# Kernel tuning notes

Hardware: AMD Instinct MI355X
Metric: run time of the kernel (lower is better)

The kernel has to match this reference:

```python
import jax, jax.numpy as jnp
import numpy as np

TAU = 0.2  # args.gumble_tau


def _segment_softmax(vals, seg, num_seg):
    # torch.sparse.softmax(dim=1): softmax over the nonzero entries of each row
    m = jax.ops.segment_max(vals, seg, num_segments=num_seg)
    e = jnp.exp(vals - m[seg])
    s = jax.ops.segment_sum(e, seg, num_segments=num_seg)
    return e / s[seg]


def _masked_attention(q_embed, k_embed, Wq, bq, Wk, bk, rows, cols, noise, num_rows):
    # Q = self.Q(q_embed); K = self.K(k_embed)
    Q = q_embed @ Wq + bq            # [Nq, H]
    K = k_embed @ Wk + bk            # [Nk, H]
    # sparse_dense_mul(adj, Q @ K.T) -> only gather edge entries (same math)
    w = jnp.sum(Q[rows] * K[cols], axis=-1)   # [E]
    g = jnp.log(-jnp.log(noise))              # gumble_G = log(-log(rand))
    z = (w - g) / TAU
    return _segment_softmax(z, rows, num_rows)


def setup_inputs() -> dict:
    key = jax.random.key(0)
    ks = jax.random.split(key, 10)
    U, I, D, H, E = 50000, 25000, 256, 128, 1600000
    inp = {
        "user_embed": jax.random.normal(ks[0], (U, D), jnp.float32),
        "item_embed": jax.random.normal(ks[1], (I, D), jnp.float32),
        "Wq": jax.random.normal(ks[2], (D, H), jnp.float32) * 0.05,
        "bq": jax.random.normal(ks[3], (H,), jnp.float32) * 0.05,
        "Wk": jax.random.normal(ks[4], (D, H), jnp.float32) * 0.05,
        "bk": jax.random.normal(ks[5], (H,), jnp.float32) * 0.05,
        "ui_rows": jax.random.randint(ks[6], (E,), 0, U, jnp.int32),
        "ui_cols": jax.random.randint(ks[7], (E,), 0, I, jnp.int32),
        "noise_ui": jax.random.uniform(ks[8], (E,), jnp.float32, 1e-6, 1.0),
        "noise_iu": jax.random.uniform(ks[9], (E,), jnp.float32, 1e-6, 1.0),
    }
    return inp


def reference(user_embed, item_embed, Wq, bq, Wk, bk, ui_rows, ui_cols, noise_ui, noise_iu):
    U = user_embed.shape[0]
    I = item_embed.shape[0]
    # M_ui: rows = users, softmax over items per user
    vals_ui = _masked_attention(user_embed, item_embed, Wq, bq, Wk, bk,
                                ui_rows, ui_cols, noise_ui, U)
    # M_iu: transposed adjacency, rows = items, same Q/K layers
    vals_iu = _masked_attention(item_embed, user_embed, Wq, bq, Wk, bk,
                                ui_cols, ui_rows, noise_iu, I)
    # mask values = cat([M_ui.values(), M_iu.values()])
    return jnp.concatenate([vals_ui, vals_iu])
```

## Files before the change

### kernel.cpp

```cpp
#include <hip/hip_runtime.h>
#include <hip/hip_fp16.h>
#include <math.h>

#define TAU_INV 5.0f
#define LOG2E   1.4426950408889634f

typedef _Float16 half2v __attribute__((ext_vector_type(2)));

__device__ __forceinline__ float fast_exp2(float x) { return __builtin_amdgcn_exp2f(x); }
__device__ __forceinline__ float fast_log2(float x) { return __builtin_amdgcn_logf(x); }

__global__ void init_sumd(double* __restrict__ seg_sumd, int n) {
    int i = blockIdx.x * blockDim.x + threadIdx.x;
    if (i < n) seg_sumd[i] = 0.0;
}

__device__ __forceinline__ double exp_double(float z) {
    float y = z * LOG2E;
    float n = rintf(y);
    float r = y - n;
    float f = fast_exp2(r);
    long long e = (long long)n + 1023;
    if (e < 1)    e = 1;
    if (e > 2046) e = 2046;
    double scale = __longlong_as_double(e << 52);
    return (double)f * scale;
}

__device__ __forceinline__ float log2_of_double(double v) {
    unsigned long long b = __double_as_longlong(v);
    int ex = (int)((b >> 52) & 0x7FFULL) - 1023;
    double m = __longlong_as_double((b & 0xFFFFFFFFFFFFFULL) | 0x3FF0000000000000ULL);
    return (float)ex + fast_log2((float)m);
}

__global__ __launch_bounds__(256) void gemm_qk_merged(
    const float* __restrict__ Xu, const float* __restrict__ Xi,
    const float* __restrict__ Wq, const float* __restrict__ bq,
    const float* __restrict__ Wk, const float* __restrict__ bk,
    __half* __restrict__ QK,
    int U, int I, int D)
{
    __shared__ float As_t[16][68];
    __shared__ float Bs_q[16][132];
    __shared__ float Bs_k[16][132];

    const int tid  = threadIdx.x;
    const int row0 = blockIdx.x * 64;
    const int tr   = tid >> 5;
    const int tc   = tid & 31;

    float4 accq[8], acck[8];
#pragma unroll
    for (int i = 0; i < 8; ++i) {
        accq[i] = make_float4(0.f, 0.f, 0.f, 0.f);
        acck[i] = make_float4(0.f, 0.f, 0.f, 0.f);
    }

    const int ar  = tid >> 2;
    const int akq = (tid & 3) * 4;

    for (int k0 = 0; k0 < D; k0 += 16) {
        {
            int gr = row0 + ar;
            float4 v = make_float4(0.f, 0.f, 0.f, 0.f);
            if (gr < U)            v = *(const float4*)&Xu[(size_t)gr * D + k0 + akq];
            else if (gr - U < I)   v = *(const float4*)&Xi[(size_t)(gr - U) * D + k0 + akq];
            As_t[akq + 0][ar] = v.x;
            As_t[akq + 1][ar] = v.y;
            As_t[akq + 2][ar] = v.z;
            As_t[akq + 3][ar] = v.w;
        }
#pragma unroll
        for (int t = 0; t < 2; ++t) {
            int idx = tid + t * 256;
            int r  = idx >> 5;
            int c4 = (idx & 31) * 4;
            float4 vq = *(const float4*)&Wq[(size_t)(k0 + r) * 128 + c4];
            float4 vk = *(const float4*)&Wk[(size_t)(k0 + r) * 128 + c4];
            *(float4*)&Bs_q[r][c4] = vq;
            *(float4*)&Bs_k[r][c4] = vk;
        }
        __syncthreads();

#pragma unroll
        for (int kk = 0; kk < 16; ++kk) {
            float4 a0  = *(const float4*)&As_t[kk][tr * 8];
            float4 a1  = *(const float4*)&As_t[kk][tr * 8 + 4];
            float4 bqv = *(const float4*)&Bs_q[kk][tc * 4];
            float4 bkv = *(const float4*)&Bs_k[kk][tc * 4];
            float a[8] = {a0.x, a0.y, a0.z, a0.w, a1.x, a1.y, a1.z, a1.w};
#pragma unroll
            for (int i = 0; i < 8; ++i) {
                accq[i].x += a[i] * bqv.x;
                accq[i].y += a[i] * bqv.y;
                accq[i].z += a[i] * bqv.z;
                accq[i].w += a[i] * bqv.w;
                acck[i].x += a[i] * bkv.x;
                acck[i].y += a[i] * bkv.y;
                acck[i].z += a[i] * bkv.z;
                acck[i].w += a[i] * bkv.w;
            }
        }
        __syncthreads();
    }

    const float4 bbq = *(const float4*)&bq[tc * 4];
    const float4 bbk = *(const float4*)&bk[tc * 4];
    const int NT = U + I;
#pragma unroll
    for (int i = 0; i < 8; ++i) {
        int gr = row0 + tr * 8 + i;
        if (gr < NT) {
            __half2 q01 = __floats2half2_rn(accq[i].x + bbq.x, accq[i].y + bbq.y);
            __half2 q23 = __floats2half2_rn(accq[i].z + bbq.z, accq[i].w + bbq.w);
            __half2 k01 = __floats2half2_rn(acck[i].x + bbk.x, acck[i].y + bbk.y);
            __half2 k23 = __floats2half2_rn(acck[i].z + bbk.z, acck[i].w + bbk.w);
            uint2 pq, pk;
            pq.x = *(const unsigned int*)&q01;
            pq.y = *(const unsigned int*)&q23;
            pk.x = *(const unsigned int*)&k01;
            pk.y = *(const unsigned int*)&k23;
            *(uint2*)&QK[(size_t)gr * 256 + tc * 4]       = pq;
            *(uint2*)&QK[(size_t)gr * 256 + 128 + tc * 4] = pk;
        }
    }
}

__global__ __launch_bounds__(256) void edge_w_both(
    const __half* __restrict__ QK,
    const int* __restrict__ rows, const int* __restrict__ cols,
    const float* __restrict__ noise_ui, const float* __restrict__ noise_iu,
    float* __restrict__ out, double* __restrict__ seg_sumd, int U, int E)
{
    const int gtid = blockIdx.x * 256 + threadIdx.x;
    const int eid  = gtid >> 3;
    if (eid >= E) return;
    const int hl = threadIdx.x & 7;

    const int r = __builtin_nontemporal_load(&rows[eid]);
    const int c = __builtin_nontemporal_load(&cols[eid]);
    const __half* urow = QK + (size_t)r * 256;
    const __half* irow = QK + (size_t)(U + c) * 256;

    const uint4 qu0 = *(const uint4*)(urow + hl * 16);
    const uint4 qu1 = *(const uint4*)(urow + hl * 16 + 8);
    const uint4 ku0 = *(const uint4*)(urow + 128 + hl * 16);
    const uint4 ku1 = *(const uint4*)(urow + 128 + hl * 16 + 8);
    const uint4 qi0 = *(const uint4*)(irow + hl * 16);
    const uint4 qi1 = *(const uint4*)(irow + hl * 16 + 8);
    const uint4 ki0 = *(const uint4*)(irow + 128 + hl * 16);
    const uint4 ki1 = *(const uint4*)(irow + 128 + hl * 16 + 8);

    float d0 = 0.0f, d1 = 0.0f;
    {
        const half2v* a0 = (const half2v*)&qu0;
        const half2v* b0 = (const half2v*)&ki0;
        const half2v* a1 = (const half2v*)&qi0;
        const half2v* b1 = (const half2v*)&ku0;
#pragma unroll
        for (int t = 0; t < 4; ++t) {
            d0 = __builtin_amdgcn_fdot2(a0[t], b0[t], d0, false);
            d1 = __builtin_amdgcn_fdot2(a1[t], b1[t], d1, false);
        }
        const half2v* a0b = (const half2v*)&qu1;
        const half2v* b0b = (const half2v*)&ki1;
        const half2v* a1b = (const half2v*)&qi1;
        const half2v* b1b = (const half2v*)&ku1;
#pragma unroll
        for (int t = 0; t < 4; ++t) {
            d0 = __builtin_amdgcn_fdot2(a0b[t], b0b[t], d0, false);
            d1 = __builtin_amdgcn_fdot2(a1b[t], b1b[t], d1, false);
        }
    }
    d0 += __shfl_xor(d0, 4);  d1 += __shfl_xor(d1, 4);
    d0 += __shfl_xor(d0, 2);  d1 += __shfl_xor(d1, 2);
    d0 += __shfl_xor(d0, 1);  d1 += __shfl_xor(d1, 1);

    if (hl < 2) {
        const int g  = hl;
        const float d  = g ? d1 : d0;
        const float nz = g ? __builtin_nontemporal_load(&noise_iu[eid])
                           : __builtin_nontemporal_load(&noise_ui[eid]);
        const float zz = (d - __logf(-__logf(nz))) * TAU_INV;
        const int s  = g ? (U + c) : r;
        __builtin_nontemporal_store(zz, &out[(size_t)g * E + eid]);
        atomicAdd(&seg_sumd[s], exp_double(zz));
    }
}

__global__ void edge_norm2v(float* __restrict__ z,
                            const int* __restrict__ rows, const int* __restrict__ cols,
                            const double* __restrict__ seg_sumd, int U, int E)
{
    int p = blockIdx.x * blockDim.x + threadIdx.x;
    int i = p * 2;
    if (i >= 2 * E) return;
    const bool iu  = (i >= E);
    const int base = iu ? (i - E) : i;
    const int off  = iu ? U : 0;
    const int* idx = iu ? cols : rows;
    int2 rc;
    rc.x = __builtin_nontemporal_load(&idx[base]);
    rc.y = __builtin_nontemporal_load(&idx[base + 1]);
    float2 zz;
    zz.x = __builtin_nontemporal_load(&z[i]);
    zz.y = __builtin_nontemporal_load(&z[i + 1]);
    float l0 = log2_of_double(seg_sumd[off + rc.x]);
    float l1 = log2_of_double(seg_sumd[off + rc.y]);
    float o0 = fast_exp2(zz.x * LOG2E - l0);
    float o1 = fast_exp2(zz.y * LOG2E - l1);
    __builtin_nontemporal_store(o0, &z[i]);
    __builtin_nontemporal_store(o1, &z[i + 1]);
}

__global__ void edge_norm2(float* __restrict__ z,
                           const int* __restrict__ rows, const int* __restrict__ cols,
                           const double* __restrict__ seg_sumd, int U, int E)
{
    int i = blockIdx.x * blockDim.x + threadIdx.x;
    if (i >= 2 * E) return;
    int s = (i < E) ? rows[i] : (U + cols[i - E]);
    float l = log2_of_double(seg_sumd[s]);
    z[i] = fast_exp2(z[i] * LOG2E - l);
}

extern "C" void kernel_launch(void* const* d_in, const int* in_sizes, int n_in,
                              void* d_out, int out_size, void* d_ws, size_t ws_size,
                              hipStream_t stream)
{
    const float* user_embed = (const float*)d_in[0];
    const float* item_embed = (const float*)d_in[1];
    const float* Wq = (const float*)d_in[2];
    const float* bq = (const float*)d_in[3];
    const float* Wk = (const float*)d_in[4];
    const float* bk = (const float*)d_in[5];
    const int* ui_rows    = (const int*)d_in[6];
    const int* ui_cols    = (const int*)d_in[7];
    const float* noise_ui = (const float*)d_in[8];
    const float* noise_iu = (const float*)d_in[9];

    const int H = in_sizes[3];
    const int D = in_sizes[2] / H;
    const int U = in_sizes[0] / D;
    const int I = in_sizes[1] / D;
    const int E = in_sizes[6];

    const int nseg = U + I;

    char* wsc = (char*)d_ws;
    __half* QK = (__half*)wsc;        wsc += (size_t)nseg * 256 * sizeof(__half);
    double* seg_sumd = (double*)wsc;  wsc += (size_t)nseg * sizeof(double);

    float* out = (float*)d_out;

    init_sumd<<<(nseg + 255) / 256, 256, 0, stream>>>(seg_sumd, nseg);

    const int gblocks = (nseg + 63) / 64;
    gemm_qk_merged<<<gblocks, 256, 0, stream>>>(user_embed, item_embed,
                                                Wq, bq, Wk, bk, QK, U, I, D);

    const int eblocks = (int)(((long long)E * 8 + 255) / 256);
    edge_w_both<<<eblocks, 256, 0, stream>>>(QK, ui_rows, ui_cols,
                                             noise_ui, noise_iu,
                                             out, seg_sumd, U, E);

    if ((E & 1) == 0) {
        const int vblocks = (E + 255) / 256;
        edge_norm2v<<<vblocks, 256, 0, stream>>>(out, ui_rows, ui_cols,
                                                 seg_sumd, U, E);
    } else {
        const int sblocks = (2 * E + 255) / 256;
        edge_norm2<<<sblocks, 256, 0, stream>>>(out, ui_rows, ui_cols,
                                                seg_sumd, U, E);
    }
}
```

Before: 485.1 us.

## Switch QK projection GEMM to split-fp16 MFMA with pre-transposed weights

Replaces the FP32 scalar-FMA tiled GEMM with an MFMA 16x16x32 fp16 kernel. Activations and weights are each split into hi and lo fp16 parts, and three MFMAs per tile approximate fp32 accuracy. A new kernel pre-transposes and splits Wq and Wk into workspace, and B fragments are read straight from global memory. It also swaps the init kernel for hipMemsetAsync and drops the nontemporal hints in edge_norm2v. The risks are extra launches, uncoalesced scalar fp16 output stores, and loss of precision from the split-fp16 approximation.

```diff
diff --git a/kernel.cpp b/kernel.cpp
--- a/kernel.cpp
+++ b/kernel.cpp
@@ -6,14 +6,11 @@
 #define LOG2E   1.4426950408889634f
 
 typedef _Float16 half2v __attribute__((ext_vector_type(2)));
+typedef _Float16 f16x8  __attribute__((ext_vector_type(8)));
+typedef float    f32x4  __attribute__((ext_vector_type(4)));
 
 __device__ __forceinline__ float fast_exp2(float x) { return __builtin_amdgcn_exp2f(x); }
 __device__ __forceinline__ float fast_log2(float x) { return __builtin_amdgcn_logf(x); }
-
-__global__ void init_sumd(double* __restrict__ seg_sumd, int n) {
-    int i = blockIdx.x * blockDim.x + threadIdx.x;
-    if (i < n) seg_sumd[i] = 0.0;
-}
 
 __device__ __forceinline__ double exp_double(float z) {
     float y = z * LOG2E;
@@ -34,95 +31,126 @@
     return (float)ex + fast_log2((float)m);
 }
 
-__global__ __launch_bounds__(256) void gemm_qk_merged(
+__global__ __launch_bounds__(256) void convert_w(
+    const float* __restrict__ Wq, const float* __restrict__ Wk,
+    _Float16* __restrict__ Wt_hi, _Float16* __restrict__ Wt_lo)
+{
+    int t = blockIdx.x * 256 + threadIdx.x;
+    int n = t >> 8;
+    int k = t & 255;
+    float x = (n < 128) ? Wq[k * 128 + n] : Wk[k * 128 + (n - 128)];
+    _Float16 hi = (_Float16)x;
+    _Float16 lo = (_Float16)(x - (float)hi);
+    Wt_hi[n * 256 + k] = hi;
+    Wt_lo[n * 256 + k] = lo;
+}
+
+__global__ __launch_bounds__(256) void gemm_qk_mfma(
     const float* __restrict__ Xu, const float* __restrict__ Xi,
-    const float* __restrict__ Wq, const float* __restrict__ bq,
-    const float* __restrict__ Wk, const float* __restrict__ bk,
-    __half* __restrict__ QK,
-    int U, int I, int D)
-{
-    __shared__ float As_t[16][68];
-    __shared__ float Bs_q[16][132];
-    __shared__ float Bs_k[16][132];
+    const _Float16* __restrict__ Wt_hi, const _Float16* __restrict__ Wt_lo,
+    const float* __restrict__ bq, const float* __restrict__ bk,
+    __half* __restrict__ QK, int U, int I)
+{
+    __shared__ _Float16 Ah[64][72];
+    __shared__ _Float16 Al[64][72];
 
     const int tid  = threadIdx.x;
     const int row0 = blockIdx.x * 64;
-    const int tr   = tid >> 5;
-    const int tc   = tid & 31;
-
-    float4 accq[8], acck[8];
-#pragma unroll
-    for (int i = 0; i < 8; ++i) {
-        accq[i] = make_float4(0.f, 0.f, 0.f, 0.f);
-        acck[i] = make_float4(0.f, 0.f, 0.f, 0.f);
-    }
-
-    const int ar  = tid >> 2;
-    const int akq = (tid & 3) * 4;
-
-    for (int k0 = 0; k0 < D; k0 += 16) {
+    const int wv   = tid >> 6;
+    const int l    = tid & 63;
+    const int lr   = l & 15;
+    const int kc   = l >> 4;
+    const int n0   = wv * 64;
+    const int NT   = U + I;
+
+    f32x4 acc[4][4];
+#pragma unroll
+    for (int i = 0; i < 4; ++i)
+#pragma unroll
+        for (int j = 0; j < 4; ++j)
+            acc[i][j] = (f32x4){0.f, 0.f, 0.f, 0.f};
+
+    const int sr = tid >> 2;
+    const int sk = (tid & 3) * 16;
+    const float* Xrow = nullptr;
+    {
+        int gr = row0 + sr;
+        if (gr < U)       Xrow = &Xu[(size_t)gr * 256];
+        else if (gr < NT) Xrow = &Xi[(size_t)(gr - U) * 256];
+    }
+
+    for (int k0 = 0; k0 < 256; k0 += 64) {
         {
-            int gr = row0 + ar;
-            float4 v = make_float4(0.f, 0.f, 0.f, 0.f);
-            if (gr < U)            v = *(const float4*)&Xu[(size_t)gr * D + k0 + akq];
-            else if (gr - U < I)   v = *(const float4*)&Xi[(size_t)(gr - U) * D + k0 + akq];
-            As_t[akq + 0][ar] = v.x;
-            As_t[akq + 1][ar] = v.y;
-            As_t[akq + 2][ar] = v.z;
-            As_t[akq + 3][ar] = v.w;
-        }
-#pragma unroll
-        for (int t = 0; t < 2; ++t) {
-            int idx = tid + t * 256;
-            int r  = idx >> 5;
-            int c4 = (idx & 31) * 4;
-            float4 vq = *(const float4*)&Wq[(size_t)(k0 + r) * 128 + c4];
-            float4 vk = *(const float4*)&Wk[(size_t)(k0 + r) * 128 + c4];
-            *(float4*)&Bs_q[r][c4] = vq;
-            *(float4*)&Bs_k[r][c4] = vk;
+            float x[16];
+            if (Xrow) {
+                float4 v0 = *(const float4*)&Xrow[k0 + sk + 0];
+                float4 v1 = *(const float4*)&Xrow[k0 + sk + 4];
+                float4 v2 = *(const float4*)&Xrow[k0 + sk + 8];
+                float4 v3 = *(const float4*)&Xrow[k0 + sk + 12];
+                x[0]=v0.x; x[1]=v0.y; x[2]=v0.z; x[3]=v0.w;
+                x[4]=v1.x; x[5]=v1.y; x[6]=v1.z; x[7]=v1.w;
+                x[8]=v2.x; x[9]=v2.y; x[10]=v2.z; x[11]=v2.w;
+                x[12]=v3.x; x[13]=v3.y; x[14]=v3.z; x[15]=v3.w;
+            } else {
+#pragma unroll
+                for (int q = 0; q < 16; ++q) x[q] = 0.f;
+            }
+            _Float16 hi[16], lo[16];
+#pragma unroll
+            for (int q = 0; q < 16; ++q) {
+                hi[q] = (_Float16)x[q];
+                lo[q] = (_Float16)(x[q] - (float)hi[q]);
+            }
+            *(f16x8*)&Ah[sr][sk]     = *(const f16x8*)&hi[0];
+            *(f16x8*)&Ah[sr][sk + 8] = *(const f16x8*)&hi[8];
+            *(f16x8*)&Al[sr][sk]     = *(const f16x8*)&lo[0];
+            *(f16x8*)&Al[sr][sk + 8] = *(const f16x8*)&lo[8];
         }
         __syncthreads();
 
 #pragma unroll
-        for (int kk = 0; kk < 16; ++kk) {
-            float4 a0  = *(const float4*)&As_t[kk][tr * 8];
-            float4 a1  = *(const float4*)&As_t[kk][tr * 8 + 4];
-            float4 bqv = *(const float4*)&Bs_q[kk][tc * 4];
-            float4 bkv = *(const float4*)&Bs_k[kk][tc * 4];
-            float a[8] = {a0.x, a0.y, a0.z, a0.w, a1.x, a1.y, a1.z, a1.w};
-#pragma unroll
-            for (int i = 0; i < 8; ++i) {
-                accq[i].x += a[i] * bqv.x;
-                accq[i].y += a[i] * bqv.y;
-                accq[i].z += a[i] * bqv.z;
-                accq[i].w += a[i] * bqv.w;
-                acck[i].x += a[i] * bkv.x;
-                acck[i].y += a[i] * bkv.y;
-                acck[i].z += a[i] * bkv.z;
-                acck[i].w += a[i] * bkv.w;
+        for (int kk = 0; kk < 2; ++kk) {
+            const int kof = kk * 32 + kc * 8;
+            f16x8 ah[4], al[4];
+#pragma unroll
+            for (int i = 0; i < 4; ++i) {
+                ah[i] = *(const f16x8*)&Ah[i * 16 + lr][kof];
+                al[i] = *(const f16x8*)&Al[i * 16 + lr][kof];
+            }
+#pragma unroll
+            for (int j = 0; j < 4; ++j) {
+                const size_t wo = (size_t)(n0 + j * 16 + lr) * 256 + k0 + kof;
+                f16x8 bh = *(const f16x8*)&Wt_hi[wo];
+                f16x8 bl = *(const f16x8*)&Wt_lo[wo];
+#pragma unroll
+                for (int i = 0; i < 4; ++i) {
+                    acc[i][j] = __builtin_amdgcn_mfma_f32_16x16x32_f16(ah[i], bh, acc[i][j], 0, 0, 0);
+                    acc[i][j] = __builtin_amdgcn_mfma_f32_16x16x32_f16(al[i], bh, acc[i][j], 0, 0, 0);
+                    acc[i][j] = __builtin_amdgcn_mfma_f32_16x16x32_f16(ah[i], bl, acc[i][j], 0, 0, 0);
+                }
             }
         }
         __syncthreads();
     }
 
-    const float4 bbq = *(const float4*)&bq[tc * 4];
-    const float4 bbk = *(const float4*)&bk[tc * 4];
-    const int NT = U + I;
-#pragma unroll
-    for (int i = 0; i < 8; ++i) {
-        int gr = row0 + tr * 8 + i;
-        if (gr < NT) {
-            __half2 q01 = __floats2half2_rn(accq[i].x + bbq.x, accq[i].y + bbq.y);
-            __half2 q23 = __floats2half2_rn(accq[i].z + bbq.z, accq[i].w + bbq.w);
-            __half2 k01 = __floats2half2_rn(acck[i].x + bbk.x, acck[i].y + bbk.y);
-            __half2 k23 = __floats2half2_rn(acck[i].z + bbk.z, acck[i].w + bbk.w);
-            uint2 pq, pk;
-            pq.x = *(const unsigned int*)&q01;
-            pq.y = *(const unsigned int*)&q23;
-            pk.x = *(const unsigned int*)&k01;
-            pk.y = *(const unsigned int*)&k23;
-            *(uint2*)&QK[(size_t)gr * 256 + tc * 4]       = pq;
-            *(uint2*)&QK[(size_t)gr * 256 + 128 + tc * 4] = pk;
+    float bias[4];
+#pragma unroll
+    for (int j = 0; j < 4; ++j) {
+        int col = n0 + j * 16 + lr;
+        bias[j] = (col < 128) ? bq[col] : bk[col - 128];
+    }
+#pragma unroll
+    for (int i = 0; i < 4; ++i) {
+#pragma unroll
+        for (int q = 0; q < 4; ++q) {
+            int gr = row0 + i * 16 + kc * 4 + q;
+            if (gr < NT) {
+#pragma unroll
+                for (int j = 0; j < 4; ++j) {
+                    int col = n0 + j * 16 + lr;
+                    QK[(size_t)gr * 256 + col] = __float2half_rn(acc[i][j][q] + bias[j]);
+                }
+            }
         }
     }
 }
@@ -200,18 +228,13 @@
     const int base = iu ? (i - E) : i;
     const int off  = iu ? U : 0;
     const int* idx = iu ? cols : rows;
-    int2 rc;
-    rc.x = __builtin_nontemporal_load(&idx[base]);
-    rc.y = __builtin_nontemporal_load(&idx[base + 1]);
-    float2 zz;
-    zz.x = __builtin_nontemporal_load(&z[i]);
-    zz.y = __builtin_nontemporal_load(&z[i + 1]);
+    int2 rc   = *(const int2*)&idx[base];
+    float2 zz = *(const float2*)&z[i];
     float l0 = log2_of_double(seg_sumd[off + rc.x]);
     float l1 = log2_of_double(seg_sumd[off + rc.y]);
     float o0 = fast_exp2(zz.x * LOG2E - l0);
     float o1 = fast_exp2(zz.y * LOG2E - l1);
-    __builtin_nontemporal_store(o0, &z[i]);
-    __builtin_nontemporal_store(o1, &z[i + 1]);
+    *(float2*)&z[i] = make_float2(o0, o1);
 }
 
 __global__ void edge_norm2(float* __restrict__ z,
@@ -249,16 +272,20 @@
     const int nseg = U + I;
 
     char* wsc = (char*)d_ws;
-    __half* QK = (__half*)wsc;        wsc += (size_t)nseg * 256 * sizeof(__half);
-    double* seg_sumd = (double*)wsc;  wsc += (size_t)nseg * sizeof(double);
+    __half* QK = (__half*)wsc;          wsc += (size_t)nseg * 256 * sizeof(__half);
+    double* seg_sumd = (double*)wsc;    wsc += (size_t)nseg * sizeof(double);
+    _Float16* Wt_hi = (_Float16*)wsc;   wsc += (size_t)256 * 256 * sizeof(_Float16);
+    _Float16* Wt_lo = (_Float16*)wsc;   wsc += (size_t)256 * 256 * sizeof(_Float16);
 
     float* out = (float*)d_out;
 
-    init_sumd<<<(nseg + 255) / 256, 256, 0, stream>>>(seg_sumd, nseg);
+    hipMemsetAsync(seg_sumd, 0, (size_t)nseg * sizeof(double), stream);
+
+    convert_w<<<256, 256, 0, stream>>>(Wq, Wk, Wt_hi, Wt_lo);
 
     const int gblocks = (nseg + 63) / 64;
-    gemm_qk_merged<<<gblocks, 256, 0, stream>>>(user_embed, item_embed,
-                                                Wq, bq, Wk, bk, QK, U, I, D);
+    gemm_qk_mfma<<<gblocks, 256, 0, stream>>>(user_embed, item_embed,
+                                              Wt_hi, Wt_lo, bq, bk, QK, U, I);
 
     const int eblocks = (int)(((long long)E * 8 + 255) / 256);
     edge_w_both<<<eblocks, 256, 0, stream>>>(QK, ui_rows, ui_cols,
```

Result: faster. 439.0 us (-9.5%).
